# Performance work log

Hardware: AMD Instinct MI355X
Metric: run time of the kernel (lower is better)

## Reference

```python
import jax, jax.numpy as jnp
import numpy as np

LOG_STD_MAX = 2.0
LOG_STD_MIN = -5.0
LN_EPS = 1e-5


def layer_norm(x, scale, bias):
    mu = jnp.mean(x, axis=-1, keepdims=True)
    var = jnp.var(x, axis=-1, keepdims=True)
    return (x - mu) * jax.lax.rsqrt(var + LN_EPS) * scale + bias


def setup_inputs() -> dict:
    key = jax.random.key(0)
    B, OBS, ACT, H, M, K = 4096, 256, 32, 512, 16, 4
    ks = jax.random.split(key, 8)
    def w(k, shape, fan_in):
        return (jax.random.normal(k, shape, jnp.float32) / np.sqrt(fan_in)).astype(jnp.float32)
    return {
        "x": jax.random.normal(ks[0], (B, OBS), jnp.float32),
        "gate_W": w(ks[1], (OBS, M), OBS),
        "gate_b": jnp.zeros((M,), jnp.float32),
        "fc1_W": w(ks[2], (OBS, H * M), OBS),
        "fc1_b": jnp.zeros((H * M,), jnp.float32),
        "norm1_scale": jnp.ones((H * M,), jnp.float32),
        "norm1_bias": jnp.zeros((H * M,), jnp.float32),
        "fc2_W": w(ks[3], (H * M, H * M), H * M),
        "fc2_b": jnp.zeros((H * M,), jnp.float32),
        "norm2_scale": jnp.ones((H * M,), jnp.float32),
        "norm2_bias": jnp.zeros((H * M,), jnp.float32),
        "mean_W": w(ks[4], (H, ACT), H),
        "mean_b": jnp.zeros((ACT,), jnp.float32),
        "logstd_W": w(ks[5], (H, ACT), H),
        "logstd_b": jnp.zeros((ACT,), jnp.float32),
        "topk": K,
    }


def reference(x, gate_W, gate_b, fc1_W, fc1_b, norm1_scale, norm1_bias,
              fc2_W, fc2_b, norm2_scale, norm2_bias,
              mean_W, mean_b, logstd_W, logstd_b, topk):
    B = x.shape[0]
    M = gate_W.shape[1]
    # gating: softmax -> topk -> renormalize -> scatter into full [B, M] scores
    gate_scores = jax.nn.softmax(x @ gate_W + gate_b, axis=-1)  # [B, M]
    topk_vals, topk_idx = jax.lax.top_k(gate_scores, topk)       # [B, K]
    topk_vals = topk_vals / jnp.sum(topk_vals, axis=-1, keepdims=True)
    scores = jnp.zeros_like(gate_scores).at[jnp.arange(B)[:, None], topk_idx].set(topk_vals)
    # trunk: Linear -> LayerNorm -> ReLU, twice
    h = jax.nn.relu(layer_norm(x @ fc1_W + fc1_b, norm1_scale, norm1_bias))
    h = jax.nn.relu(layer_norm(h @ fc2_W + fc2_b, norm2_scale, norm2_bias))
    # reshape [B, H*M] -> [B, H, M] (expert m = strided slice), weighted MEAN over experts
    h = h.reshape(B, -1, M)                                      # [B, H, M]
    mixed = jnp.einsum('bhm,bm->bh', h, scores) / M              # mean, not sum
    mean = mixed @ mean_W + mean_b
    log_std = jnp.tanh(mixed @ logstd_W + logstd_b)
    log_std = LOG_STD_MIN + 0.5 * (LOG_STD_MAX - LOG_STD_MIN) * (log_std + 1.0)
    return mean, log_std
```

## Files before the change

kernel.cpp:

```cpp
#include <hip/hip_runtime.h>
#include <hip/hip_bf16.h>

typedef unsigned int u32;
typedef unsigned short u16;
typedef __bf16 bf16x8 __attribute__((ext_vector_type(8)));
typedef float f32x4 __attribute__((ext_vector_type(4)));

__device__ __forceinline__ u16 f2b(float f) {
    __bf16 b = (__bf16)f;
    return __builtin_bit_cast(u16, b);
}

__device__ __forceinline__ void gld_lds16(const void* g, void* l) {
    __builtin_amdgcn_global_load_lds(
        (const __attribute__((address_space(1))) u32*)(size_t)g,
        (__attribute__((address_space(3))) u32*)(u32)(size_t)l,
        16, 0, 0);
}

#define BARRIER __builtin_amdgcn_s_barrier()
#define LGKM0 asm volatile("s_waitcnt lgkmcnt(0)" ::: "memory")
#define VMC6 asm volatile("s_waitcnt vmcnt(6)" ::: "memory")
#define VMC0 asm volatile("s_waitcnt vmcnt(0)" ::: "memory")
#define MFMA16(d, a, b) d = __builtin_amdgcn_mfma_f32_16x16x32_bf16(a, b, d, 0, 0, 0)

__global__ __launch_bounds__(256) void cast_bf16_kernel(
    const float* __restrict__ in, u16* __restrict__ out, int n4)
{
    int i = blockIdx.x * 256 + threadIdx.x;
    if (i < n4) {
        float4 f = reinterpret_cast<const float4*>(in)[i];
        u32 lo = (u32)f2b(f.x) | ((u32)f2b(f.y) << 16);
        u32 hi = (u32)f2b(f.z) | ((u32)f2b(f.w) << 16);
        uint2 o; o.x = lo; o.y = hi;
        reinterpret_cast<uint2*>(out)[i] = o;
    }
}

__global__ __launch_bounds__(256) void transpose_cast_kernel(
    const float* __restrict__ in, u16* __restrict__ out, int R, int C)
{
    __shared__ float tile[64][65];
    const int t = threadIdx.x;
    const int c0 = blockIdx.x * 64;
    const int r0 = blockIdx.y * 64;
    #pragma unroll
    for (int i = 0; i < 16; ++i) {
        int idx = t + i * 256;
        int r = idx >> 6, c = idx & 63;
        tile[r][c] = in[(long)(r0 + r) * C + (c0 + c)];
    }
    __syncthreads();
    #pragma unroll
    for (int i = 0; i < 8; ++i) {
        int idx = t + i * 256;
        int rr = idx >> 5;
        int cc = idx & 31;
        u32 p = (u32)f2b(tile[cc * 2 + 0][rr]) | ((u32)f2b(tile[cc * 2 + 1][rr]) << 16);
        *reinterpret_cast<u32*>(&out[(long)(c0 + rr) * R + r0 + cc * 2]) = p;
    }
}

__global__ __launch_bounds__(256) void gate_kernel(
    const float* __restrict__ x, const float* __restrict__ gW,
    const float* __restrict__ gb, const int* __restrict__ topk,
    float* __restrict__ scores)
{
    const int t = threadIdx.x;
    const int row = blockIdx.x * 4 + (t >> 6);
    const int l = t & 63;
    const int m = l & 15;
    const int q = l >> 4;
    const int Kk = *topk;
    const float* xr = x + (long)row * 256;
    float p = 0.f;
    for (int k = q * 64; k < q * 64 + 64; ++k)
        p += xr[k] * gW[k * 16 + m];
    p += __shfl_xor(p, 16);
    p += __shfl_xor(p, 32);
    float logit = p + gb[m];
    float mx = logit;
    #pragma unroll
    for (int d = 1; d < 16; d <<= 1) mx = fmaxf(mx, __shfl_xor(mx, d));
    int rank = 0;
    #pragma unroll
    for (int j = 0; j < 16; ++j) {
        float vj = __shfl(logit, (l & 48) | j);
        rank += (vj > logit) || (vj == logit && j < m);
    }
    bool sel = rank < Kk;
    float e = sel ? expf(logit - mx) : 0.f;
    float ssum = e;
    #pragma unroll
    for (int d = 1; d < 16; d <<= 1) ssum += __shfl_xor(ssum, d);
    if (q == 0) scores[row * 16 + m] = e / ssum;
}


template<int GRAN>
__device__ __forceinline__ void stage_half(
    const u16* __restrict__ src, int ld, int rowbase, int kk,
    u16* ldsregion, int h, int w, int l)
{
    #pragma unroll
    for (int j = 0; j < 2; ++j) {
        const int c = w * 2 + j;
        const int o = c * 1024 + l * 16;
        const int os = o ^ (((o >> 7) & 7) << 4);
        const int pos = o >> 7;
        const int row = ((pos / GRAN) * 2 + h) * GRAN + (pos & (GRAN - 1));
        const u16* g = src + (long)(rowbase + row) * ld + kk + ((os & 127) >> 1);
        gld_lds16(g, ldsregion + c * 512);
    }
}

__device__ __forceinline__ bf16x8 ldfrag(const u16* region, int pos, int col) {
    const int o = (pos * 128 + col * 2) ^ ((pos & 7) << 4);
    return *reinterpret_cast<const bf16x8*>(reinterpret_cast<const char*>(region) + o);
}

template<int CB>
__device__ __forceinline__ void ktile_group(
    const u16* __restrict__ A, int lda, const u16* __restrict__ BT, int ldb,
    int brow, int bcol, int kkA1, int kkR,
    int wr, int wc, int r4, int q8, int w, int l,
    u16 (&lds)[2][4][8192], f32x4 (&acc)[8][4])
{
    bf16x8 aL[4][2], aH[4][2], bL[2][2], bH[2][2];

    #pragma unroll
    for (int m = 0; m < 4; ++m) {
        aL[m][0] = ldfrag(lds[CB][0], wr * 64 + m * 16 + r4, q8);
        aL[m][1] = ldfrag(lds[CB][0], wr * 64 + m * 16 + r4, 32 + q8);
    }
    #pragma unroll
    for (int n = 0; n < 2; ++n) {
        bL[n][0] = ldfrag(lds[CB][2], wc * 32 + n * 16 + r4, q8);
        bL[n][1] = ldfrag(lds[CB][2], wc * 32 + n * 16 + r4, 32 + q8);
    }
    stage_half<64>(A, lda, brow, kkA1, &lds[1 - CB][1][0], 1, w, l);
    BARRIER; LGKM0;
    __builtin_amdgcn_s_setprio(1);
    #pragma unroll
    for (int m = 0; m < 4; ++m)
        #pragma unroll
        for (int n = 0; n < 2; ++n) {
            MFMA16(acc[m][n], aL[m][0], bL[n][0]);
            MFMA16(acc[m][n], aL[m][1], bL[n][1]);
        }
    __builtin_amdgcn_s_setprio(0);
    BARRIER;

    #pragma unroll
    for (int n = 0; n < 2; ++n) {
        bH[n][0] = ldfrag(lds[CB][3], wc * 32 + n * 16 + r4, q8);
        bH[n][1] = ldfrag(lds[CB][3], wc * 32 + n * 16 + r4, 32 + q8);
    }
    stage_half<64>(A, lda, brow, kkR, &lds[CB][0][0], 0, w, l);
    BARRIER; LGKM0;
    __builtin_amdgcn_s_setprio(1);
    #pragma unroll
    for (int m = 0; m < 4; ++m)
        #pragma unroll
        for (int n = 0; n < 2; ++n) {
            MFMA16(acc[m][2 + n], aL[m][0], bH[n][0]);
            MFMA16(acc[m][2 + n], aL[m][1], bH[n][1]);
        }
    __builtin_amdgcn_s_setprio(0);
    BARRIER;

    #pragma unroll
    for (int m = 0; m < 4; ++m) {
        aH[m][0] = ldfrag(lds[CB][1], wr * 64 + m * 16 + r4, q8);
        aH[m][1] = ldfrag(lds[CB][1], wr * 64 + m * 16 + r4, 32 + q8);
    }
    stage_half<32>(BT, ldb, bcol, kkR, &lds[CB][2][0], 0, w, l);
    BARRIER; LGKM0;
    __builtin_amdgcn_s_setprio(1);
    #pragma unroll
    for (int m = 0; m < 4; ++m)
        #pragma unroll
        for (int n = 0; n < 2; ++n) {
            MFMA16(acc[4 + m][2 + n], aH[m][0], bH[n][0]);
            MFMA16(acc[4 + m][2 + n], aH[m][1], bH[n][1]);
        }
    __builtin_amdgcn_s_setprio(0);
    BARRIER;

    stage_half<32>(BT, ldb, bcol, kkR, &lds[CB][3][0], 1, w, l);
    BARRIER;
    __builtin_amdgcn_s_setprio(1);
    #pragma unroll
    for (int m = 0; m < 4; ++m)
        #pragma unroll
        for (int n = 0; n < 2; ++n) {
            MFMA16(acc[4 + m][n], aH[m][0], bL[n][0]);
            MFMA16(acc[4 + m][n], aH[m][1], bL[n][1]);
        }
    __builtin_amdgcn_s_setprio(0);
    VMC6;
    BARRIER;
}

__global__ __launch_bounds__(512, 2) void gemm256(
    const u16* __restrict__ A, int lda,
    const u16* __restrict__ BT, int ldb,
    float* __restrict__ C, int ldc, int K)
{
    __shared__ __align__(16) u16 lds[2][4][8192];
    const int t = threadIdx.x;
    const int w = t >> 6, l = t & 63;
    const int wr = w >> 2, wc = w & 3;
    const int r4 = l & 15, q8 = (l >> 4) * 8;
    const int brow = blockIdx.y * 256, bcol = blockIdx.x * 256;
    const int NT = K >> 6;

    f32x4 acc[8][4];
    #pragma unroll
    for (int m = 0; m < 8; ++m)
        #pragma unroll
        for (int n = 0; n < 4; ++n)
            acc[m][n] = (f32x4){0.f, 0.f, 0.f, 0.f};

    stage_half<64>(A, lda, brow, 0, &lds[0][0][0], 0, w, l);
    stage_half<32>(BT, ldb, bcol, 0, &lds[0][2][0], 0, w, l);
    stage_half<32>(BT, ldb, bcol, 0, &lds[0][3][0], 1, w, l);
    stage_half<64>(A, lda, brow, 0, &lds[0][1][0], 1, w, l);
    stage_half<64>(A, lda, brow, 64, &lds[1][0][0], 0, w, l);
    stage_half<32>(BT, ldb, bcol, 64, &lds[1][2][0], 0, w, l);
    stage_half<32>(BT, ldb, bcol, 64, &lds[1][3][0], 1, w, l);
    VMC6;
    BARRIER;

    for (int i = 0; i < (NT >> 1); ++i) {
        const int U = 2 * i;
        int tV = U + 1;
        int tU2 = U + 2;
        int tV2 = U + 3;
        if (tU2 >= NT) tU2 -= NT;
        if (tV2 >= NT) tV2 -= NT;
        const int kkV = (tV >= NT ? tV - NT : tV) << 6;
        const int kkU2 = tU2 << 6;
        const int kkV2 = tV2 << 6;

        ktile_group<0>(A, lda, BT, ldb, brow, bcol, kkV, kkU2,
                       wr, wc, r4, q8, w, l, lds, acc);
        ktile_group<1>(A, lda, BT, ldb, brow, bcol, kkU2, kkV2,
                       wr, wc, r4, q8, w, l, lds, acc);
    }

    VMC0;

    const int crow0 = (l >> 4) * 4;
    const int ccol = l & 15;
    #pragma unroll
    for (int m = 0; m < 8; ++m) {
        #pragma unroll
        for (int n = 0; n < 4; ++n) {
            int gr = brow + wr * 128 + m * 16 + crow0;
            int gc = bcol + wc * 64 + n * 16 + ccol;
            #pragma unroll
            for (int r = 0; r < 4; ++r)
                C[(long)(gr + r) * ldc + gc] = acc[m][n][r];
        }
    }
}

__global__ __launch_bounds__(256) void ln1_kernel(
    const float* __restrict__ Y, const float* __restrict__ fcb,
    const float* __restrict__ g, const float* __restrict__ be,
    u16* __restrict__ H)
{
    const int N = 8192;
    const int row = blockIdx.x;
    const int t = threadIdx.x;
    const float* y = Y + (long)row * N;
    const int base = t * 32;
    float v[32];
    float s = 0.f, s2 = 0.f;
    #pragma unroll
    for (int j = 0; j < 8; ++j) {
        float4 f = *reinterpret_cast<const float4*>(y + base + j * 4);
        float4 bb = *reinterpret_cast<const float4*>(fcb + base + j * 4);
        float a0 = f.x + bb.x, a1 = f.y + bb.y, a2 = f.z + bb.z, a3 = f.w + bb.w;
        v[j * 4 + 0] = a0; v[j * 4 + 1] = a1; v[j * 4 + 2] = a2; v[j * 4 + 3] = a3;
        s += a0 + a1 + a2 + a3;
        s2 += a0 * a0 + a1 * a1 + a2 * a2 + a3 * a3;
    }
    #pragma unroll
    for (int d = 32; d > 0; d >>= 1) { s += __shfl_down(s, d); s2 += __shfl_down(s2, d); }
    __shared__ float red[8];
    if ((t & 63) == 0) { red[t >> 6] = s; red[4 + (t >> 6)] = s2; }
    __syncthreads();
    s = red[0] + red[1] + red[2] + red[3];
    s2 = red[4] + red[5] + red[6] + red[7];
    float mu = s * (1.f / N);
    float var = s2 * (1.f / N) - mu * mu;
    float rs = rsqrtf(var + 1e-5f);
    __align__(16) u16 o[32];
    #pragma unroll
    for (int i = 0; i < 32; ++i) {
        float z = (v[i] - mu) * rs * g[base + i] + be[base + i];
        o[i] = f2b(fmaxf(z, 0.f));
    }
    u16* h = H + (long)row * N + base;
    #pragma unroll
    for (int j = 0; j < 4; ++j)
        *reinterpret_cast<uint4*>(h + j * 8) = *reinterpret_cast<const uint4*>(&o[j * 8]);
}

__global__ __launch_bounds__(256) void ln2_mix_kernel(
    const float* __restrict__ Y, const float* __restrict__ fcb,
    const float* __restrict__ g, const float* __restrict__ be,
    const float* __restrict__ scores, float* __restrict__ mixed)
{
    const int N = 8192;
    const int row = blockIdx.x;
    const int t = threadIdx.x;
    const float* y = Y + (long)row * N;
    const int base = t * 32;
    __shared__ float sc[16];
    if (t < 16) sc[t] = scores[row * 16 + t];
    float v[32];
    float s = 0.f, s2 = 0.f;
    #pragma unroll
    for (int j = 0; j < 8; ++j) {
        float4 f = *reinterpret_cast<const float4*>(y + base + j * 4);
        float4 bb = *reinterpret_cast<const float4*>(fcb + base + j * 4);
        float a0 = f.x + bb.x, a1 = f.y + bb.y, a2 = f.z + bb.z, a3 = f.w + bb.w;
        v[j * 4 + 0] = a0; v[j * 4 + 1] = a1; v[j * 4 + 2] = a2; v[j * 4 + 3] = a3;
        s += a0 + a1 + a2 + a3;
        s2 += a0 * a0 + a1 * a1 + a2 * a2 + a3 * a3;
    }
    #pragma unroll
    for (int d = 32; d > 0; d >>= 1) { s += __shfl_down(s, d); s2 += __shfl_down(s2, d); }
    __shared__ float red[8];
    if ((t & 63) == 0) { red[t >> 6] = s; red[4 + (t >> 6)] = s2; }
    __syncthreads();
    s = red[0] + red[1] + red[2] + red[3];
    s2 = red[4] + red[5] + red[6] + red[7];
    float mu = s * (1.f / N);
    float var = s2 * (1.f / N) - mu * mu;
    float rs = rsqrtf(var + 1e-5f);
    float m0 = 0.f, m1 = 0.f;
    #pragma unroll
    for (int m = 0; m < 16; ++m) {
        float z0 = fmaxf((v[m] - mu) * rs * g[base + m] + be[base + m], 0.f);
        float z1 = fmaxf((v[16 + m] - mu) * rs * g[base + 16 + m] + be[base + 16 + m], 0.f);
        m0 += z0 * sc[m];
        m1 += z1 * sc[m];
    }
    float2 out; out.x = m0 * (1.f / 16.f); out.y = m1 * (1.f / 16.f);
    *reinterpret_cast<float2*>(&mixed[(long)row * 512 + 2 * t]) = out;
}

__global__ __launch_bounds__(256) void heads_kernel(
    const float* __restrict__ mixed, const float* __restrict__ mW,
    const float* __restrict__ mb, const float* __restrict__ sW,
    const float* __restrict__ sb, float* __restrict__ out)
{
    const int B = 4096;
    const int rb = blockIdx.x * 8;
    const int t = threadIdx.x;
    const int bl = t >> 5;
    const int a = t & 31;
    __shared__ float mx[8][512];
    for (int i = t; i < 8 * 512; i += 256)
        mx[i >> 9][i & 511] = mixed[(long)(rb + (i >> 9)) * 512 + (i & 511)];
    __syncthreads();
    float am = mb[a], as = sb[a];
    for (int h = 0; h < 512; ++h) {
        float xv = mx[bl][h];
        am += xv * mW[h * 32 + a];
        as += xv * sW[h * 32 + a];
    }
    int row = rb + bl;
    out[(long)row * 32 + a] = am;
    float ts = tanhf(as);
    out[(long)B * 32 + (long)row * 32 + a] = -5.0f + 3.5f * (ts + 1.0f);
}

extern "C" void kernel_launch(void* const* d_in, const int* in_sizes, int n_in,
                              void* d_out, int out_size, void* d_ws, size_t ws_size,
                              hipStream_t stream) {
    const float* x   = (const float*)d_in[0];
    const float* gW  = (const float*)d_in[1];
    const float* gb  = (const float*)d_in[2];
    const float* w1  = (const float*)d_in[3];
    const float* b1  = (const float*)d_in[4];
    const float* g1  = (const float*)d_in[5];
    const float* be1 = (const float*)d_in[6];
    const float* w2  = (const float*)d_in[7];
    const float* b2  = (const float*)d_in[8];
    const float* g2  = (const float*)d_in[9];
    const float* be2 = (const float*)d_in[10];
    const float* mW  = (const float*)d_in[11];
    const float* mb  = (const float*)d_in[12];
    const float* sW  = (const float*)d_in[13];
    const float* sb  = (const float*)d_in[14];
    const int* topk  = (const int*)d_in[15];
    float* out = (float*)d_out;

    char* ws = (char*)d_ws;
    u16* W2T = (u16*)ws;            ws += (long)8192 * 8192 * 2;
    float* Y = (float*)ws;          ws += (long)4096 * 8192 * 4;
    u16* H1 = (u16*)ws;             ws += (long)4096 * 8192 * 2;
    u16* W1T = (u16*)ws;            ws += (long)8192 * 256 * 2;
    u16* XB = (u16*)ws;             ws += (long)4096 * 256 * 2;
    float* SCR = (float*)ws;        ws += (long)4096 * 16 * 4;
    float* MIX = (float*)ws;        ws += (long)4096 * 512 * 4;

    cast_bf16_kernel<<<1024, 256, 0, stream>>>(x, XB, 262144);
    transpose_cast_kernel<<<dim3(128, 4), 256, 0, stream>>>(w1, W1T, 256, 8192);
    transpose_cast_kernel<<<dim3(128, 128), 256, 0, stream>>>(w2, W2T, 8192, 8192);
    gate_kernel<<<1024, 256, 0, stream>>>(x, gW, gb, topk, SCR);

    gemm256<<<dim3(32, 16), 512, 0, stream>>>(XB, 256, W1T, 256, Y, 8192, 256);
    ln1_kernel<<<4096, 256, 0, stream>>>(Y, b1, g1, be1, H1);

    gemm256<<<dim3(32, 16), 512, 0, stream>>>(H1, 8192, W2T, 8192, Y, 8192, 8192);
    ln2_mix_kernel<<<4096, 256, 0, stream>>>(Y, b2, g2, be2, SCR, MIX);

    heads_kernel<<<512, 256, 0, stream>>>(MIX, mW, mb, sW, sb, out);
}
```

Baseline: 767.7 us.

## Store GEMM outputs as bf16, remap blocks per XCD, add partial LDS wait

```diff
diff --git a/kernel.cpp b/kernel.cpp
--- a/kernel.cpp
+++ b/kernel.cpp
@@ -9,6 +9,10 @@
 __device__ __forceinline__ u16 f2b(float f) {
     __bf16 b = (__bf16)f;
     return __builtin_bit_cast(u16, b);
+}
+__device__ __forceinline__ float b2f(u16 v) {
+    u32 x = ((u32)v) << 16;
+    return __builtin_bit_cast(float, x);
 }
 
 __device__ __forceinline__ void gld_lds16(const void* g, void* l) {
@@ -20,6 +24,7 @@
 
 #define BARRIER __builtin_amdgcn_s_barrier()
 #define LGKM0 asm volatile("s_waitcnt lgkmcnt(0)" ::: "memory")
+#define LGKM8 asm volatile("s_waitcnt lgkmcnt(8)" ::: "memory")
 #define VMC6 asm volatile("s_waitcnt vmcnt(6)" ::: "memory")
 #define VMC0 asm volatile("s_waitcnt vmcnt(0)" ::: "memory")
 #define MFMA16(d, a, b) d = __builtin_amdgcn_mfma_f32_16x16x32_bf16(a, b, d, 0, 0, 0)
@@ -139,6 +144,7 @@
         bL[n][1] = ldfrag(lds[CB][2], wc * 32 + n * 16 + r4, 32 + q8);
     }
     stage_half<64>(A, lda, brow, kkA1, &lds[1 - CB][1][0], 1, w, l);
+    LGKM8;
     BARRIER; LGKM0;
     __builtin_amdgcn_s_setprio(1);
     #pragma unroll
@@ -205,14 +211,18 @@
 __global__ __launch_bounds__(512, 2) void gemm256(
     const u16* __restrict__ A, int lda,
     const u16* __restrict__ BT, int ldb,
-    float* __restrict__ C, int ldc, int K)
+    u16* __restrict__ C, int ldc, int K)
 {
     __shared__ __align__(16) u16 lds[2][4][8192];
     const int t = threadIdx.x;
     const int w = t >> 6, l = t & 63;
     const int wr = w >> 2, wc = w & 3;
     const int r4 = l & 15, q8 = (l >> 4) * 8;
-    const int brow = blockIdx.y * 256, bcol = blockIdx.x * 256;
+    const int bid = blockIdx.y * 32 + blockIdx.x;
+    const int xcd = bid & 7, within = bid >> 3;
+    const int by = (xcd >> 2) * 8 + (within >> 3);
+    const int bx = (xcd & 3) * 8 + (within & 7);
+    const int brow = by * 256, bcol = bx * 256;
     const int NT = K >> 6;
 
     f32x4 acc[8][4];
@@ -261,31 +271,35 @@
             int gc = bcol + wc * 64 + n * 16 + ccol;
             #pragma unroll
             for (int r = 0; r < 4; ++r)
-                C[(long)(gr + r) * ldc + gc] = acc[m][n][r];
+                C[(long)(gr + r) * ldc + gc] = f2b(acc[m][n][r]);
         }
     }
 }
 
 __global__ __launch_bounds__(256) void ln1_kernel(
-    const float* __restrict__ Y, const float* __restrict__ fcb,
+    const u16* __restrict__ Y, const float* __restrict__ fcb,
     const float* __restrict__ g, const float* __restrict__ be,
     u16* __restrict__ H)
 {
     const int N = 8192;
     const int row = blockIdx.x;
     const int t = threadIdx.x;
-    const float* y = Y + (long)row * N;
+    const u16* y = Y + (long)row * N;
     const int base = t * 32;
     float v[32];
     float s = 0.f, s2 = 0.f;
     #pragma unroll
-    for (int j = 0; j < 8; ++j) {
-        float4 f = *reinterpret_cast<const float4*>(y + base + j * 4);
-        float4 bb = *reinterpret_cast<const float4*>(fcb + base + j * 4);
-        float a0 = f.x + bb.x, a1 = f.y + bb.y, a2 = f.z + bb.z, a3 = f.w + bb.w;
-        v[j * 4 + 0] = a0; v[j * 4 + 1] = a1; v[j * 4 + 2] = a2; v[j * 4 + 3] = a3;
-        s += a0 + a1 + a2 + a3;
-        s2 += a0 * a0 + a1 * a1 + a2 * a2 + a3 * a3;
+    for (int j = 0; j < 4; ++j) {
+        uint4 q = *reinterpret_cast<const uint4*>(y + base + j * 8);
+        const u32 ww[4] = {q.x, q.y, q.z, q.w};
+        #pragma unroll
+        for (int e = 0; e < 4; ++e) {
+            float a0 = b2f((u16)(ww[e] & 0xffff)) + fcb[base + j * 8 + e * 2];
+            float a1 = b2f((u16)(ww[e] >> 16)) + fcb[base + j * 8 + e * 2 + 1];
+            v[j * 8 + e * 2] = a0; v[j * 8 + e * 2 + 1] = a1;
+            s += a0 + a1;
+            s2 += a0 * a0 + a1 * a1;
+        }
     }
     #pragma unroll
     for (int d = 32; d > 0; d >>= 1) { s += __shfl_down(s, d); s2 += __shfl_down(s2, d); }
@@ -310,27 +324,31 @@
 }
 
 __global__ __launch_bounds__(256) void ln2_mix_kernel(
-    const float* __restrict__ Y, const float* __restrict__ fcb,
+    const u16* __restrict__ Y, const float* __restrict__ fcb,
     const float* __restrict__ g, const float* __restrict__ be,
     const float* __restrict__ scores, float* __restrict__ mixed)
 {
     const int N = 8192;
     const int row = blockIdx.x;
     const int t = threadIdx.x;
-    const float* y = Y + (long)row * N;
+    const u16* y = Y + (long)row * N;
     const int base = t * 32;
     __shared__ float sc[16];
     if (t < 16) sc[t] = scores[row * 16 + t];
     float v[32];
     float s = 0.f, s2 = 0.f;
     #pragma unroll
-    for (int j = 0; j < 8; ++j) {
-        float4 f = *reinterpret_cast<const float4*>(y + base + j * 4);
-        float4 bb = *reinterpret_cast<const float4*>(fcb + base + j * 4);
-        float a0 = f.x + bb.x, a1 = f.y + bb.y, a2 = f.z + bb.z, a3 = f.w + bb.w;
-        v[j * 4 + 0] = a0; v[j * 4 + 1] = a1; v[j * 4 + 2] = a2; v[j * 4 + 3] = a3;
-        s += a0 + a1 + a2 + a3;
-        s2 += a0 * a0 + a1 * a1 + a2 * a2 + a3 * a3;
+    for (int j = 0; j < 4; ++j) {
+        uint4 q = *reinterpret_cast<const uint4*>(y + base + j * 8);
+        const u32 ww[4] = {q.x, q.y, q.z, q.w};
+        #pragma unroll
+        for (int e = 0; e < 4; ++e) {
+            float a0 = b2f((u16)(ww[e] & 0xffff)) + fcb[base + j * 8 + e * 2];
+            float a1 = b2f((u16)(ww[e] >> 16)) + fcb[base + j * 8 + e * 2 + 1];
+            v[j * 8 + e * 2] = a0; v[j * 8 + e * 2 + 1] = a1;
+            s += a0 + a1;
+            s2 += a0 * a0 + a1 * a1;
+        }
     }
     #pragma unroll
     for (int d = 32; d > 0; d >>= 1) { s += __shfl_down(s, d); s2 += __shfl_down(s2, d); }
@@ -403,7 +421,7 @@
 
     char* ws = (char*)d_ws;
     u16* W2T = (u16*)ws;            ws += (long)8192 * 8192 * 2;
-    float* Y = (float*)ws;          ws += (long)4096 * 8192 * 4;
+    u16* Yb = (u16*)ws;             ws += (long)4096 * 8192 * 2;
     u16* H1 = (u16*)ws;             ws += (long)4096 * 8192 * 2;
     u16* W1T = (u16*)ws;            ws += (long)8192 * 256 * 2;
     u16* XB = (u16*)ws;             ws += (long)4096 * 256 * 2;
@@ -415,11 +433,11 @@
     transpose_cast_kernel<<<dim3(128, 128), 256, 0, stream>>>(w2, W2T, 8192, 8192);
     gate_kernel<<<1024, 256, 0, stream>>>(x, gW, gb, topk, SCR);
 
-    gemm256<<<dim3(32, 16), 512, 0, stream>>>(XB, 256, W1T, 256, Y, 8192, 256);
-    ln1_kernel<<<4096, 256, 0, stream>>>(Y, b1, g1, be1, H1);
-
-    gemm256<<<dim3(32, 16), 512, 0, stream>>>(H1, 8192, W2T, 8192, Y, 8192, 8192);
-    ln2_mix_kernel<<<4096, 256, 0, stream>>>(Y, b2, g2, be2, SCR, MIX);
+    gemm256<<<dim3(32, 16), 512, 0, stream>>>(XB, 256, W1T, 256, Yb, 8192, 256);
+    ln1_kernel<<<4096, 256, 0, stream>>>(Yb, b1, g1, be1, H1);
+
+    gemm256<<<dim3(32, 16), 512, 0, stream>>>(H1, 8192, W2T, 8192, Yb, 8192, 8192);
+    ln2_mix_kernel<<<4096, 256, 0, stream>>>(Yb, b2, g2, be2, SCR, MIX);
 
     heads_kernel<<<512, 256, 0, stream>>>(MIX, mW, mb, sW, sb, out);
 }
```

Measured after the change: 718.7 us. 1.07x faster.
